# Kernel optimization log

Measured on AMD Instinct MI355X. Metric: run time of the kernel, lower is better.

Reference implementation:

```python
import jax, jax.numpy as jnp
import numpy as np

LAMBD = 0.1  # lambd from __init__

N_POINTS = 262144
D_EMBED = 512
N_CLUSTERS = 64


def setup_inputs() -> dict:
    key = jax.random.key(0)
    k1, k2 = jax.random.split(key)
    x = jax.random.normal(k1, (N_POINTS, D_EMBED), dtype=jnp.float32)
    # original init: uniform(-1, 1)
    centroids = jax.random.uniform(k2, (N_CLUSTERS, D_EMBED), dtype=jnp.float32, minval=-1.0, maxval=1.0)
    return {"x": x, "centroids": centroids, "alpha": 100}


def reference(x, centroids, alpha):
    # stack_dist[i, n] = sum_d (x[n,d] - centroids[i,d])^2, fused via the
    x2 = jnp.sum(x * x, axis=1)                      # [N]
    c2 = jnp.sum(centroids * centroids, axis=1)      # [k]
    cross = jnp.einsum('nd,kd->kn', x, centroids)    # [k, N]
    dist = x2[None, :] + c2[:, None] - 2.0 * cross   # [k, N]
    # exp(-alpha*(dist - min)) / sum == softmax(-alpha*dist) along the k axis
    soft = jax.nn.softmax(-jnp.float32(alpha) * dist, axis=0)  # [k, N]
    k_means_loss = LAMBD * jnp.mean(jnp.sum(dist * soft, axis=0))
    return k_means_loss
```

## Files before the change

### kernel.cpp

```cpp
#include <hip/hip_runtime.h>
#include <hip/hip_bf16.h>

#define N_POINTS   262144
#define D_EMBED    512
#define N_CLUSTERS 64
#define LAMBD      0.1f

#define PTS_PER_WAVE  32
#define PTS_PER_BLK   128

typedef __attribute__((ext_vector_type(8)))  short short8;
typedef __attribute__((ext_vector_type(16))) float f32x16;

__device__ __forceinline__ unsigned short f2bf(float f) {
    union { float f; unsigned u; } v; v.f = f;
    unsigned u = v.u;
    return (unsigned short)((u + 0x7FFFu + ((u >> 16) & 1u)) >> 16);
}

__global__ void prep_kernel(const float* __restrict__ cent,
                            float* __restrict__ c2_ws,
                            unsigned short* __restrict__ afrag,
                            float* __restrict__ out) {
    const int k    = blockIdx.x;
    const int lane = threadIdx.x;
    const float* row = cent + (size_t)k * D_EMBED;

    float4 v0 = ((const float4*)row)[lane * 2 + 0];
    float4 v1 = ((const float4*)row)[lane * 2 + 1];

    float s = v0.x*v0.x + v0.y*v0.y + v0.z*v0.z + v0.w*v0.w
            + v1.x*v1.x + v1.y*v1.y + v1.z*v1.z + v1.w*v1.w;
    #pragma unroll
    for (int m = 1; m < 64; m <<= 1) s += __shfl_xor(s, m);
    if (lane == 0) c2_ws[k] = s;

    const int st = lane >> 1;
    const int h  = lane & 1;
    const int t  = k >> 5;
    const int m  = k & 31;
    const size_t idx8 = ((size_t)(st * 2 + t) * 64 + m + 32 * h) * 8;

    ushort4 h0, h1;
    h0.x = f2bf(v0.x); h0.y = f2bf(v0.y); h0.z = f2bf(v0.z); h0.w = f2bf(v0.w);
    h1.x = f2bf(v1.x); h1.y = f2bf(v1.y); h1.z = f2bf(v1.z); h1.w = f2bf(v1.w);
    *(ushort4*)&afrag[idx8 + 0] = h0;
    *(ushort4*)&afrag[idx8 + 4] = h1;

    if (k == 0 && lane == 0) *out = 0.0f;
}

__global__ __launch_bounds__(256, 2)
void main_kernel(const float* __restrict__ x,
                 const int* __restrict__ alpha_p,
                 const float* __restrict__ c2_ws,
                 const unsigned short* __restrict__ afrag,
                 float* __restrict__ out) {
    __shared__ unsigned short alds[64 * 64 * 8];
    __shared__ float c2s[N_CLUSTERS];
    __shared__ float bsum[4];

    const int tid  = threadIdx.x;
    const int lane = tid & 63;
    const int w    = tid >> 6;

    #pragma unroll
    for (int it = 0; it < 16; ++it) {
        const int e8 = it * 256 + tid;
        *(short8*)&alds[(size_t)e8 * 8] = *(const short8*)&afrag[(size_t)e8 * 8];
    }
    if (tid < 64) c2s[tid] = c2_ws[tid];
    __syncthreads();

    const float alpha = (float)alpha_p[0];
    const int n = lane & 31;
    const int h = lane >> 5;
    const size_t pt = (size_t)blockIdx.x * PTS_PER_BLK + w * PTS_PER_WAVE + n;
    const float* xp = x + pt * D_EMBED + 8 * h;

    f32x16 acc0, acc1;
    #pragma unroll
    for (int r = 0; r < 16; ++r) { acc0[r] = 0.0f; acc1[r] = 0.0f; }

    float4 buf[2][16];
    #pragma unroll
    for (int i = 0; i < 8; ++i) {
        buf[0][2*i+0] = *(const float4*)(xp + 16 * i);
        buf[0][2*i+1] = *(const float4*)(xp + 16 * i + 4);
    }

    float x2 = 0.0f;
    #pragma unroll
    for (int g = 0; g < 4; ++g) {
        const int cb = g & 1, nb = cb ^ 1;
        if (g < 3) {
            #pragma unroll
            for (int i = 0; i < 8; ++i) {
                const int s = (g + 1) * 8 + i;
                buf[nb][2*i+0] = *(const float4*)(xp + 16 * s);
                buf[nb][2*i+1] = *(const float4*)(xp + 16 * s + 4);
            }
        }
        #pragma unroll
        for (int i = 0; i < 8; ++i) {
            const int s = g * 8 + i;
            const float4 u0 = buf[cb][2*i+0];
            const float4 u1 = buf[cb][2*i+1];

            x2 += u0.x*u0.x + u0.y*u0.y + u0.z*u0.z + u0.w*u0.w
                + u1.x*u1.x + u1.y*u1.y + u1.z*u1.z + u1.w*u1.w;

            short8 b;
            b[0] = (short)f2bf(u0.x); b[1] = (short)f2bf(u0.y);
            b[2] = (short)f2bf(u0.z); b[3] = (short)f2bf(u0.w);
            b[4] = (short)f2bf(u1.x); b[5] = (short)f2bf(u1.y);
            b[6] = (short)f2bf(u1.z); b[7] = (short)f2bf(u1.w);

            short8 a0 = *(const short8*)&alds[((size_t)(s * 2 + 0) * 64 + lane) * 8];
            short8 a1 = *(const short8*)&alds[((size_t)(s * 2 + 1) * 64 + lane) * 8];

            acc0 = __builtin_amdgcn_mfma_f32_32x32x16_bf16(a0, b, acc0, 0, 0, 0);
            acc1 = __builtin_amdgcn_mfma_f32_32x32x16_bf16(a1, b, acc1, 0, 0, 0);
        }
    }
    x2 += __shfl_xor(x2, 32);

    float minv = 1e30f;
    #pragma unroll
    for (int r = 0; r < 16; ++r) {
        const int rr = (r & 3) + 8 * (r >> 2) + 4 * h;
        const float d0 = x2 + c2s[rr]      - 2.0f * acc0[r];
        const float d1 = x2 + c2s[rr + 32] - 2.0f * acc1[r];
        acc0[r] = d0; acc1[r] = d1;
        minv = fminf(minv, fminf(d0, d1));
    }
    minv = fminf(minv, __shfl_xor(minv, 32));

    float esum = 0.0f, wsum = 0.0f;
    #pragma unroll
    for (int r = 0; r < 16; ++r) {
        const float e0 = __expf(-alpha * (acc0[r] - minv));
        const float e1 = __expf(-alpha * (acc1[r] - minv));
        esum += e0 + e1;
        wsum += acc0[r] * e0 + acc1[r] * e1;
    }
    esum += __shfl_xor(esum, 32);
    wsum += __shfl_xor(wsum, 32);

    float pv = wsum / esum;
    #pragma unroll
    for (int m = 1; m < 64; m <<= 1) pv += __shfl_xor(pv, m);

    if (lane == 0) bsum[w] = pv;
    __syncthreads();
    if (tid == 0) {
        const float T = bsum[0] + bsum[1] + bsum[2] + bsum[3];
        atomicAdd(out, T * (LAMBD / (2.0f * (float)N_POINTS)));
    }
}

extern "C" void kernel_launch(void* const* d_in, const int* in_sizes, int n_in,
                              void* d_out, int out_size, void* d_ws, size_t ws_size,
                              hipStream_t stream) {
    const float* x      = (const float*)d_in[0];
    const float* cent   = (const float*)d_in[1];
    const int*   alphap = (const int*)d_in[2];
    float* out = (float*)d_out;

    float*          c2_ws = (float*)d_ws;
    unsigned short* afrag = (unsigned short*)((char*)d_ws + 256);

    hipLaunchKernelGGL(prep_kernel, dim3(N_CLUSTERS), dim3(64), 0, stream,
                       cent, c2_ws, afrag, out);
    hipLaunchKernelGGL(main_kernel, dim3(N_POINTS / PTS_PER_BLK), dim3(256), 0, stream,
                       x, alphap, c2_ws, afrag, out);
}
```

Measured before the change: 677.7 us.

## Stage x tiles through swizzled LDS double buffer with coalesced loads

Each block now handles 256 points with 512 threads. Threads cooperatively load contiguous 64-float chunks of x with coalesced float4 reads, convert them to bf16 and write them into a swizzled, double-buffered LDS tile. Each wave then reads its MFMA B operands from LDS instead of strided per-lane global loads. Per-point squared norms are reduced via shuffles into shared memory. This aims to improve global load coalescing for the memory-bound x stream, at the cost of more LDS traffic and a block-wide barrier per chunk.

Result: slower. 710.9 us (+4.9%).

```diff
diff --git a/kernel.cpp b/kernel.cpp
--- a/kernel.cpp
+++ b/kernel.cpp
@@ -6,8 +6,11 @@
 #define N_CLUSTERS 64
 #define LAMBD      0.1f
 
-#define PTS_PER_WAVE  32
-#define PTS_PER_BLK   128
+#define THREADS      512
+#define PTS_PER_BLK  256
+#define PTS_PER_WAVE 32
+#define KC           64
+#define NCHUNK       (D_EMBED / KC)
 
 typedef __attribute__((ext_vector_type(8)))  short short8;
 typedef __attribute__((ext_vector_type(16))) float f32x16;
@@ -50,99 +53,128 @@
     if (k == 0 && lane == 0) *out = 0.0f;
 }
 
-__global__ __launch_bounds__(256, 2)
+__global__ __launch_bounds__(THREADS, 2)
 void main_kernel(const float* __restrict__ x,
                  const int* __restrict__ alpha_p,
                  const float* __restrict__ c2_ws,
                  const unsigned short* __restrict__ afrag,
                  float* __restrict__ out) {
     __shared__ unsigned short alds[64 * 64 * 8];
+    __shared__ unsigned short xb[2][PTS_PER_BLK * KC];
+    __shared__ float x2a[PTS_PER_BLK];
     __shared__ float c2s[N_CLUSTERS];
-    __shared__ float bsum[4];
+    __shared__ float bsum[8];
 
     const int tid  = threadIdx.x;
     const int lane = tid & 63;
     const int w    = tid >> 6;
 
     #pragma unroll
-    for (int it = 0; it < 16; ++it) {
-        const int e8 = it * 256 + tid;
+    for (int it = 0; it < 8; ++it) {
+        const int e8 = it * THREADS + tid;
         *(short8*)&alds[(size_t)e8 * 8] = *(const short8*)&afrag[(size_t)e8 * 8];
     }
     if (tid < 64) c2s[tid] = c2_ws[tid];
-    __syncthreads();
+
+    const int pt0 = tid >> 4;
+    const int gf  = tid & 15;
+    const char* src0 = (const char*)x
+        + (size_t)blockIdx.x * PTS_PER_BLK * (D_EMBED * 4)
+        + (size_t)pt0 * (D_EMBED * 4) + gf * 16;
+    const int soff = pt0 * KC + (((gf >> 1) ^ (pt0 & 7)) * 8) + (gf & 1) * 4;
 
     const float alpha = (float)alpha_p[0];
-    const int n = lane & 31;
-    const int h = lane >> 5;
-    const size_t pt = (size_t)blockIdx.x * PTS_PER_BLK + w * PTS_PER_WAVE + n;
-    const float* xp = x + pt * D_EMBED + 8 * h;
+    const int n    = lane & 31;
+    const int h    = lane >> 5;
+    const int pl   = w * PTS_PER_WAVE + n;
+    const int xrow = pl * KC;
+    const int xswz = pl & 7;
 
     f32x16 acc0, acc1;
     #pragma unroll
-    for (int r = 0; r < 16; ++r) { acc0[r] = 0.0f; acc1[r] = 0.0f; }
-
-    float4 buf[2][16];
+    for (int q = 0; q < 16; ++q) { acc0[q] = 0.0f; acc1[q] = 0.0f; }
+
+    float4 r[8];
+    float  x2p[8];
+    #pragma unroll
+    for (int i = 0; i < 8; ++i) x2p[i] = 0.0f;
+
+    #pragma unroll
+    for (int i = 0; i < 8; ++i)
+        r[i] = *(const float4*)(src0 + (size_t)i * (32 * D_EMBED * 4));
+    __syncthreads();
     #pragma unroll
     for (int i = 0; i < 8; ++i) {
-        buf[0][2*i+0] = *(const float4*)(xp + 16 * i);
-        buf[0][2*i+1] = *(const float4*)(xp + 16 * i + 4);
-    }
-
-    float x2 = 0.0f;
-    #pragma unroll
-    for (int g = 0; g < 4; ++g) {
-        const int cb = g & 1, nb = cb ^ 1;
-        if (g < 3) {
+        const float4 u = r[i];
+        x2p[i] += u.x*u.x + u.y*u.y + u.z*u.z + u.w*u.w;
+        ushort4 hv;
+        hv.x = f2bf(u.x); hv.y = f2bf(u.y); hv.z = f2bf(u.z); hv.w = f2bf(u.w);
+        *(ushort4*)&xb[0][soff + i * (32 * KC)] = hv;
+    }
+    __syncthreads();
+
+    int cur = 0;
+    #pragma unroll
+    for (int c = 0; c < NCHUNK; ++c) {
+        if (c + 1 < NCHUNK) {
             #pragma unroll
-            for (int i = 0; i < 8; ++i) {
-                const int s = (g + 1) * 8 + i;
-                buf[nb][2*i+0] = *(const float4*)(xp + 16 * s);
-                buf[nb][2*i+1] = *(const float4*)(xp + 16 * s + 4);
-            }
+            for (int i = 0; i < 8; ++i)
+                r[i] = *(const float4*)(src0 + (size_t)i * (32 * D_EMBED * 4)
+                                             + (size_t)(c + 1) * (KC * 4));
         }
         #pragma unroll
-        for (int i = 0; i < 8; ++i) {
-            const int s = g * 8 + i;
-            const float4 u0 = buf[cb][2*i+0];
-            const float4 u1 = buf[cb][2*i+1];
-
-            x2 += u0.x*u0.x + u0.y*u0.y + u0.z*u0.z + u0.w*u0.w
-                + u1.x*u1.x + u1.y*u1.y + u1.z*u1.z + u1.w*u1.w;
-
-            short8 b;
-            b[0] = (short)f2bf(u0.x); b[1] = (short)f2bf(u0.y);
-            b[2] = (short)f2bf(u0.z); b[3] = (short)f2bf(u0.w);
-            b[4] = (short)f2bf(u1.x); b[5] = (short)f2bf(u1.y);
-            b[6] = (short)f2bf(u1.z); b[7] = (short)f2bf(u1.w);
-
-            short8 a0 = *(const short8*)&alds[((size_t)(s * 2 + 0) * 64 + lane) * 8];
-            short8 a1 = *(const short8*)&alds[((size_t)(s * 2 + 1) * 64 + lane) * 8];
-
+        for (int s = 0; s < 4; ++s) {
+            const int S = c * 4 + s;
+            const short8 b  = *(const short8*)&xb[cur][xrow + (((2 * s + h) ^ xswz) * 8)];
+            const short8 a0 = *(const short8*)&alds[((size_t)(S * 2 + 0) * 64 + lane) * 8];
+            const short8 a1 = *(const short8*)&alds[((size_t)(S * 2 + 1) * 64 + lane) * 8];
             acc0 = __builtin_amdgcn_mfma_f32_32x32x16_bf16(a0, b, acc0, 0, 0, 0);
             acc1 = __builtin_amdgcn_mfma_f32_32x32x16_bf16(a1, b, acc1, 0, 0, 0);
         }
-    }
-    x2 += __shfl_xor(x2, 32);
+        if (c + 1 < NCHUNK) {
+            #pragma unroll
+            for (int i = 0; i < 8; ++i) {
+                const float4 u = r[i];
+                x2p[i] += u.x*u.x + u.y*u.y + u.z*u.z + u.w*u.w;
+                ushort4 hv;
+                hv.x = f2bf(u.x); hv.y = f2bf(u.y); hv.z = f2bf(u.z); hv.w = f2bf(u.w);
+                *(ushort4*)&xb[cur ^ 1][soff + i * (32 * KC)] = hv;
+            }
+        }
+        __syncthreads();
+        cur ^= 1;
+    }
+
+    #pragma unroll
+    for (int i = 0; i < 8; ++i) {
+        float v = x2p[i];
+        v += __shfl_xor(v, 1);
+        v += __shfl_xor(v, 2);
+        v += __shfl_xor(v, 4);
+        v += __shfl_xor(v, 8);
+        if ((tid & 15) == 0) x2a[pt0 + 32 * i] = v;
+    }
+    __syncthreads();
+    const float x2 = x2a[pl];
 
     float minv = 1e30f;
     #pragma unroll
-    for (int r = 0; r < 16; ++r) {
-        const int rr = (r & 3) + 8 * (r >> 2) + 4 * h;
-        const float d0 = x2 + c2s[rr]      - 2.0f * acc0[r];
-        const float d1 = x2 + c2s[rr + 32] - 2.0f * acc1[r];
-        acc0[r] = d0; acc1[r] = d1;
+    for (int q = 0; q < 16; ++q) {
+        const int rr = (q & 3) + 8 * (q >> 2) + 4 * h;
+        const float d0 = x2 + c2s[rr]      - 2.0f * acc0[q];
+        const float d1 = x2 + c2s[rr + 32] - 2.0f * acc1[q];
+        acc0[q] = d0; acc1[q] = d1;
         minv = fminf(minv, fminf(d0, d1));
     }
     minv = fminf(minv, __shfl_xor(minv, 32));
 
     float esum = 0.0f, wsum = 0.0f;
     #pragma unroll
-    for (int r = 0; r < 16; ++r) {
-        const float e0 = __expf(-alpha * (acc0[r] - minv));
-        const float e1 = __expf(-alpha * (acc1[r] - minv));
+    for (int q = 0; q < 16; ++q) {
+        const float e0 = __expf(-alpha * (acc0[q] - minv));
+        const float e1 = __expf(-alpha * (acc1[q] - minv));
         esum += e0 + e1;
-        wsum += acc0[r] * e0 + acc1[r] * e1;
+        wsum += acc0[q] * e0 + acc1[q] * e1;
     }
     esum += __shfl_xor(esum, 32);
     wsum += __shfl_xor(wsum, 32);
@@ -154,7 +186,9 @@
     if (lane == 0) bsum[w] = pv;
     __syncthreads();
     if (tid == 0) {
-        const float T = bsum[0] + bsum[1] + bsum[2] + bsum[3];
+        float T = 0.0f;
+        #pragma unroll
+        for (int i = 0; i < 8; ++i) T += bsum[i];
         atomicAdd(out, T * (LAMBD / (2.0f * (float)N_POINTS)));
     }
 }
@@ -172,6 +206,6 @@
 
     hipLaunchKernelGGL(prep_kernel, dim3(N_CLUSTERS), dim3(64), 0, stream,
                        cent, c2_ws, afrag, out);
-    hipLaunchKernelGGL(main_kernel, dim3(N_POINTS / PTS_PER_BLK), dim3(256), 0, stream,
+    hipLaunchKernelGGL(main_kernel, dim3(N_POINTS / PTS_PER_BLK), dim3(THREADS), 0, stream,
                        x, alphap, c2_ws, afrag, out);
 }
```
